# Kernel tuning notes

Hardware: AMD Instinct MI355X
Metric: run time of the kernel (lower is better)

The kernel has to match this reference:

```python
import jax, jax.numpy as jnp
import numpy as np

B, C, H, W = 8, 3, 224, 224
OC, NQ, DEPTH, HID = 64, 16, 2, 256
DIM = 2 ** NQ  # 65536: size of the quantum state vector / probs


def setup_inputs() -> dict:
    key = jax.random.key(0)
    ks = jax.random.split(key, 6)
    return {
        "x": jax.random.normal(ks[0], (B, C, H, W), jnp.float32),
        # measure_proj = Linear(DIM, 256) -> ReLU -> Linear(256, OC)
        "W1": jax.random.normal(ks[1], (HID, DIM), jnp.float32) / np.sqrt(DIM).astype(np.float32),
        "b1": jax.random.normal(ks[2], (HID,), jnp.float32) * 0.01,
        "W2": jax.random.normal(ks[3], (OC, HID), jnp.float32) / np.sqrt(HID).astype(np.float32),
        "b2": jax.random.normal(ks[4], (OC,), jnp.float32) * 0.01,
        # variational circuit params: declared in the module but never used by the math
        "params": jax.random.normal(ks[5], (OC, DEPTH, NQ, 3), jnp.float32),
    }


def reference(x, W1, b1, W2, b2, params):
    """Faithful vectorization of QuantumConv2DLayer.forward.

    _encode_2d ignores the patch and always returns the |0> state; _apply_circuit
    is identity. Hence probs = one_hot(0, DIM) for every (b, oc, i, j), and each
    output entry equals sum(measure_proj(one_hot(0))) — a single scalar broadcast
    over [B, OC, H, W]. Linear(one_hot(0)) selects column 0 of W1.
    """
    b, _, h, w = x.shape
    oc = W2.shape[0]
    hidden = jax.nn.relu(W1[:, 0] + b1)          # [HID]
    val = jnp.sum(W2 @ hidden + b2)              # scalar: .sum() over out_channels
    return jnp.broadcast_to(val, (b, oc, h, w))  # [B, OC, H, W]
```

## Files before the change

kernel.cpp:

```cpp
#include <hip/hip_runtime.h>


#define DIM   65536
#define HID   256
#define OC_N  64
#define OUT_N (8ULL * 64 * 224 * 224)

__global__ void compute_val_kernel(const float* __restrict__ W1,
                                   const float* __restrict__ b1,
                                   const float* __restrict__ W2,
                                   const float* __restrict__ b2,
                                   float* __restrict__ ws) {
    const int h = threadIdx.x;

    float hidden = W1[(size_t)h * DIM] + b1[h];
    hidden = hidden > 0.0f ? hidden : 0.0f;

    float colsum = 0.0f;
#pragma unroll
    for (int oc = 0; oc < OC_N; ++oc) {
        colsum += W2[oc * HID + h];
    }

    float partial = hidden * colsum + (h < OC_N ? b2[h] : 0.0f);

#pragma unroll
    for (int off = 32; off > 0; off >>= 1) {
        partial += __shfl_down(partial, off, 64);
    }

    __shared__ float smem[4];
    if ((h & 63) == 0) smem[h >> 6] = partial;
    __syncthreads();
    if (h == 0) {
        ws[0] = smem[0] + smem[1] + smem[2] + smem[3];
    }
}

__global__ void fill_out_kernel(const float* __restrict__ ws,
                                float4* __restrict__ out) {
    const float v = ws[0];
    const float4 v4 = make_float4(v, v, v, v);
    const size_t n4 = OUT_N / 4;
    const size_t stride = (size_t)gridDim.x * blockDim.x;
    for (size_t i = (size_t)blockIdx.x * blockDim.x + threadIdx.x; i < n4; i += stride) {
        out[i] = v4;
    }
}

extern "C" void kernel_launch(void* const* d_in, const int* in_sizes, int n_in,
                              void* d_out, int out_size, void* d_ws, size_t ws_size,
                              hipStream_t stream) {
    const float* W1 = (const float*)d_in[1];
    const float* b1 = (const float*)d_in[2];
    const float* W2 = (const float*)d_in[3];
    const float* b2 = (const float*)d_in[4];
    float* out = (float*)d_out;
    float* ws  = (float*)d_ws;

    compute_val_kernel<<<1, 256, 0, stream>>>(W1, b1, W2, b2, ws);

    fill_out_kernel<<<2048, 256, 0, stream>>>(ws, (float4*)out);
}
```

Measured before the change: 154.4 us.

## Fuse scalar computation into fill kernel with nontemporal contiguous stores

Merges the single-block scalar reduction kernel and the broadcast fill kernel into one launch. Every block recomputes the scalar redundantly from W1, b1, W2 and b2, which removes a kernel launch and the dependency through workspace memory. The fill loop changes from a grid-stride pattern to contiguous per-block chunks and uses nontemporal stores. The trade-off is redundant reads of W2 and the strided W1 column in every block, which should mostly hit in cache.

```diff
diff --git a/kernel.cpp b/kernel.cpp
--- a/kernel.cpp
+++ b/kernel.cpp
@@ -5,24 +5,28 @@
 #define HID   256
 #define OC_N  64
 #define OUT_N (8ULL * 64 * 224 * 224)
+#define NBLK  2048
 
-__global__ void compute_val_kernel(const float* __restrict__ W1,
-                                   const float* __restrict__ b1,
-                                   const float* __restrict__ W2,
-                                   const float* __restrict__ b2,
-                                   float* __restrict__ ws) {
-    const int h = threadIdx.x;
+typedef float f32x4 __attribute__((ext_vector_type(4)));
 
-    float hidden = W1[(size_t)h * DIM] + b1[h];
+__global__ void __launch_bounds__(256, 8)
+fused_fill_kernel(const float* __restrict__ W1,
+                  const float* __restrict__ b1,
+                  const float* __restrict__ W2,
+                  const float* __restrict__ b2,
+                  f32x4* __restrict__ out) {
+    const int t = threadIdx.x;
+
+    float hidden = W1[(size_t)t * DIM] + b1[t];
     hidden = hidden > 0.0f ? hidden : 0.0f;
 
     float colsum = 0.0f;
 #pragma unroll
     for (int oc = 0; oc < OC_N; ++oc) {
-        colsum += W2[oc * HID + h];
+        colsum += W2[oc * HID + t];
     }
 
-    float partial = hidden * colsum + (h < OC_N ? b2[h] : 0.0f);
+    float partial = hidden * colsum + (t < OC_N ? b2[t] : 0.0f);
 
 #pragma unroll
     for (int off = 32; off > 0; off >>= 1) {
@@ -30,21 +34,21 @@
     }
 
     __shared__ float smem[4];
-    if ((h & 63) == 0) smem[h >> 6] = partial;
+    __shared__ float s_val;
+    if ((t & 63) == 0) smem[t >> 6] = partial;
     __syncthreads();
-    if (h == 0) {
-        ws[0] = smem[0] + smem[1] + smem[2] + smem[3];
-    }
-}
+    if (t == 0) s_val = smem[0] + smem[1] + smem[2] + smem[3];
+    __syncthreads();
 
-__global__ void fill_out_kernel(const float* __restrict__ ws,
-                                float4* __restrict__ out) {
-    const float v = ws[0];
-    const float4 v4 = make_float4(v, v, v, v);
+    const float v = s_val;
+    f32x4 v4 = {v, v, v, v};
+
     const size_t n4 = OUT_N / 4;
-    const size_t stride = (size_t)gridDim.x * blockDim.x;
-    for (size_t i = (size_t)blockIdx.x * blockDim.x + threadIdx.x; i < n4; i += stride) {
-        out[i] = v4;
+    const size_t per_blk = (n4 + NBLK - 1) / NBLK;
+    const size_t begin = (size_t)blockIdx.x * per_blk;
+    const size_t end = begin + per_blk < n4 ? begin + per_blk : n4;
+    for (size_t i = begin + t; i < end; i += 256) {
+        __builtin_nontemporal_store(v4, &out[i]);
     }
 }
 
@@ -55,10 +59,6 @@
     const float* b1 = (const float*)d_in[2];
     const float* W2 = (const float*)d_in[3];
     const float* b2 = (const float*)d_in[4];
-    float* out = (float*)d_out;
-    float* ws  = (float*)d_ws;
 
-    compute_val_kernel<<<1, 256, 0, stream>>>(W1, b1, W2, b2, ws);
-
-    fill_out_kernel<<<2048, 256, 0, stream>>>(ws, (float4*)out);
+    fused_fill_kernel<<<NBLK, 256, 0, stream>>>(W1, b1, W2, b2, (f32x4*)d_out);
 }
```

Measured after the change: 175.4 us. 13.6% more time.
